# Performance work log

Measured on AMD Instinct MI355X. Metric: run time of the kernel, lower is better.

The kernel has to match this reference:

```python
import jax, jax.numpy as jnp
import numpy as np

B, F, D, H = 2048, 32, 64, 64

def setup_inputs() -> dict:
    key = jax.random.key(0)
    k1, k2, k3 = jax.random.split(key, 3)
    x = jax.random.normal(k1, (B, F, D), dtype=jnp.float32)
    W1 = jax.random.normal(k2, (D, H), dtype=jnp.float32) * 0.01
    b1 = jnp.zeros((H,), dtype=jnp.float32)
    Ws = jax.random.normal(k3, (H, 1), dtype=jnp.float32) * 0.01
    bs = jnp.zeros((1,), dtype=jnp.float32)
    return {"x": x, "W1": W1, "b1": b1, "Ws": Ws, "bs": bs}

def reference(x, W1, b1, Ws, bs):
    # pairwise field interactions: cross[b, p, d] = x[b, i_p, d] * x[b, j_p, d]
    f = x.shape[1]
    ii, jj = np.triu_indices(f, k=1)  # P = f*(f-1)/2 pairs
    cross = x[:, ii, :] * x[:, jj, :]            # [B, P, D]
    # small MLP (DNN with one hidden layer, relu, dropout disabled in eval)
    h = jax.nn.relu(jnp.einsum('bpd,dh->bph', cross, W1) + b1)  # [B, P, H]
    # attention score per pair, softmax over pairs
    scores = (jnp.einsum('bph,ho->bpo', h, Ws) + bs).squeeze(-1)  # [B, P]
    attn = jax.nn.softmax(scores, axis=-1)                        # [B, P]
    pool = jnp.sum(cross * attn[:, :, None], axis=1)              # [B, D]
    afm = jnp.sum(pool, axis=1, keepdims=True)                    # [B, 1]
    return afm
```

## Files before the change

kernel.cpp:

```cpp
#include <hip/hip_runtime.h>


#define F 32
#define D 64
#define H 64
#define P 496
#define MT 32
#define RB 72

typedef __attribute__((ext_vector_type(8))) _Float16 f16x8;
typedef __attribute__((ext_vector_type(2))) _Float16 f16x2;
typedef __attribute__((ext_vector_type(4))) float f32x4;
typedef __attribute__((ext_vector_type(2))) float f32x2;

__global__ __launch_bounds__(256, 4) void afm_kernel(
    const float* __restrict__ x, const float* __restrict__ W1,
    const float* __restrict__ b1, const float* __restrict__ Ws,
    const float* __restrict__ bs, float* __restrict__ out)
{
    __shared__ _Float16 xs[F * RB];
    __shared__ _Float16 w1f[4096];
    __shared__ float2 bw[H];
    __shared__ int pairtab[512];
    __shared__ float rednum[4], redden[4];

    const int tid  = threadIdx.x;
    const int b    = blockIdx.x;
    const int lane = tid & 63;
    const int wid  = tid >> 6;
    const int l15  = lane & 15;
    const int quad = lane >> 4;

    const float4* xb4 = (const float4*)(x + (size_t)b * (F * D));
    for (int v = tid; v < (F * D) / 4; v += 256) {
        float4 w = xb4[v];
        int row = v >> 4, col = (v & 15) * 4;
        f16x2 lo = { (_Float16)w.x, (_Float16)w.y };
        f16x2 hi = { (_Float16)w.z, (_Float16)w.w };
        *(f16x2*)&xs[row * RB + col]     = lo;
        *(f16x2*)&xs[row * RB + col + 2] = hi;
    }
    const float4* w14 = (const float4*)W1;
    #pragma unroll
    for (int s = 0; s < 4; ++s) {
        int v = tid + s * 256;
        float4 w = w14[v];
        int k  = v >> 4;
        int ks = k >> 5, kq = (k >> 3) & 3, j8 = k & 7;
        int n0 = (v & 15) * 4;
        float e4[4] = { w.x, w.y, w.z, w.w };
        #pragma unroll
        for (int c = 0; c < 4; ++c) {
            int n = n0 + c, nt = n >> 4, l = n & 15;
            w1f[(((ks * 4 + nt) * 16 + l) * 4 + kq) * 8 + j8] = (_Float16)e4[c];
        }
    }
    if (tid < H) bw[tid] = make_float2(b1[tid], Ws[tid]);
    for (int p = tid; p < 512; p += 256) {
        int i, j;
        if (p < P) {
            i = (int)((63.0f - __builtin_sqrtf((float)(3969 - 8 * p))) * 0.5f);
            if (i * (63 - i) / 2 > p) --i;
            if ((i + 1) * (62 - i) / 2 <= p) ++i;
            j = i + 1 + (p - i * (63 - i) / 2);
        } else { i = 0; j = 0; }
        pairtab[p] = (i * RB * 2) << 16 | (j * RB * 2);
    }
    const float bsv = bs[0];
    __syncthreads();

    f16x8 wfrag[4][2];
    #pragma unroll
    for (int nt = 0; nt < 4; ++nt)
        #pragma unroll
        for (int ks = 0; ks < 2; ++ks)
            wfrag[nt][ks] = *(const f16x8*)&w1f[(((ks * 4 + nt) * 16 + l15) * 4 + quad) * 8];

    const _Float16 onev = (l15 == 0) ? (_Float16)1.0f : (_Float16)0.0f;
    const f16x8 onesf = {onev, onev, onev, onev, onev, onev, onev, onev};

    f32x2 b2[8], w2[8];
    #pragma unroll
    for (int nt = 0; nt < 4; ++nt) {
        const float2* src = &bw[nt * 16 + quad * 4];
        float2 q0 = src[0], q1 = src[1], q2 = src[2], q3 = src[3];
        b2[nt*2+0] = (f32x2){q0.x, q1.x}; w2[nt*2+0] = (f32x2){q0.y, q1.y};
        b2[nt*2+1] = (f32x2){q2.x, q3.x}; w2[nt*2+1] = (f32x2){q2.y, q3.y};
    }

    const char* xsb = (const char*)xs;
    const int qb = quad << 4;
    float num = 0.f, den = 0.f;
    const f32x2 z2 = {0.f, 0.f};

    for (int t = wid; t < MT; t += 4) {
        const int p0 = t * 16;
        const int pk = pairtab[p0 + l15];
        const int io = ((unsigned)pk) >> 16;
        const int jo = pk & 0xFFFF;

        f16x8 xi0 = *(const f16x8*)(xsb + io + qb);
        f16x8 xj0 = *(const f16x8*)(xsb + jo + qb);
        f16x8 xi1 = *(const f16x8*)(xsb + io + 64 + qb);
        f16x8 xj1 = *(const f16x8*)(xsb + jo + 64 + qb);

        f16x8 A0 = xi0 * xj0;
        f16x8 A1 = xi1 * xj1;

        f32x4 acc[4];
        #pragma unroll
        for (int nt = 0; nt < 4; ++nt) { f32x4 z = {0.f,0.f,0.f,0.f}; acc[nt] = z; }
        f32x4 accs = {0.f, 0.f, 0.f, 0.f};

        #pragma unroll
        for (int nt = 0; nt < 4; ++nt)
            acc[nt] = __builtin_amdgcn_mfma_f32_16x16x32_f16(wfrag[nt][0], A0, acc[nt], 0, 0, 0);
        accs = __builtin_amdgcn_mfma_f32_16x16x32_f16(onesf, A0, accs, 0, 0, 0);
        #pragma unroll
        for (int nt = 0; nt < 4; ++nt)
            acc[nt] = __builtin_amdgcn_mfma_f32_16x16x32_f16(wfrag[nt][1], A1, acc[nt], 0, 0, 0);
        accs = __builtin_amdgcn_mfma_f32_16x16x32_f16(onesf, A1, accs, 0, 0, 0);

        f32x2 s2 = {0.f, 0.f};
        #pragma unroll
        for (int nt = 0; nt < 4; ++nt) {
            f32x2 lo = {acc[nt][0], acc[nt][1]};
            f32x2 hi = {acc[nt][2], acc[nt][3]};
            lo += b2[nt*2+0]; hi += b2[nt*2+1];
            lo = __builtin_elementwise_max(lo, z2);
            hi = __builtin_elementwise_max(hi, z2);
            s2 = lo * w2[nt*2+0] + s2;
            s2 = hi * w2[nt*2+1] + s2;
        }
        float s = s2.x + s2.y;
        s += __shfl_xor(s, 16, 64);
        s += __shfl_xor(s, 32, 64);

        float e = __expf(s + bsv);
        e = (quad == 0 && p0 + l15 < P) ? e : 0.f;
        num = fmaf(e, accs[0], num);
        den += e;
    }

    #pragma unroll
    for (int off = 8; off >= 1; off >>= 1) {
        num += __shfl_xor(num, off, 64);
        den += __shfl_xor(den, off, 64);
    }
    if (lane == 0) { rednum[wid] = num; redden[wid] = den; }
    __syncthreads();
    if (tid == 0) {
        float nn = rednum[0] + rednum[1] + rednum[2] + rednum[3];
        float dd = redden[0] + redden[1] + redden[2] + redden[3];
        out[b] = nn / dd;
    }
}

extern "C" void kernel_launch(void* const* d_in, const int* in_sizes, int n_in,
                              void* d_out, int out_size, void* d_ws, size_t ws_size,
                              hipStream_t stream) {
    const float* x  = (const float*)d_in[0];
    const float* W1 = (const float*)d_in[1];
    const float* b1 = (const float*)d_in[2];
    const float* Ws = (const float*)d_in[3];
    const float* bs = (const float*)d_in[4];
    float* out = (float*)d_out;
    const int B = in_sizes[0] / (F * D);
    afm_kernel<<<B, 256, 0, stream>>>(x, W1, b1, Ws, bs, out);
}
```

Baseline: 86.77 us.

## Process two batch rows per block to amortize weight and pair-table setup

Each block now handles two batch samples. It stages both x slices in shared memory and loops over 64 pair tiles instead of 32, so the W1 fp16 relayout, bias loads and pair-index table are built once per two samples. The bs bias is dropped from the exponent, relying on softmax shift invariance. The grid is halved, which reduces parallelism but still fills the GPU. The change also assumes B is divisible by two.

```diff
diff --git a/kernel.cpp b/kernel.cpp
--- a/kernel.cpp
+++ b/kernel.cpp
@@ -5,8 +5,8 @@
 #define D 64
 #define H 64
 #define P 496
-#define MT 32
 #define RB 72
+#define G 2
 
 typedef __attribute__((ext_vector_type(8))) _Float16 f16x8;
 typedef __attribute__((ext_vector_type(2))) _Float16 f16x2;
@@ -18,27 +18,30 @@
     const float* __restrict__ b1, const float* __restrict__ Ws,
     const float* __restrict__ bs, float* __restrict__ out)
 {
-    __shared__ _Float16 xs[F * RB];
+    __shared__ _Float16 xs[G][F * RB];
     __shared__ _Float16 w1f[4096];
     __shared__ float2 bw[H];
     __shared__ int pairtab[512];
-    __shared__ float rednum[4], redden[4];
+    __shared__ float rednum[G][4], redden[G][4];
 
     const int tid  = threadIdx.x;
-    const int b    = blockIdx.x;
     const int lane = tid & 63;
     const int wid  = tid >> 6;
     const int l15  = lane & 15;
     const int quad = lane >> 4;
+    const int b0   = blockIdx.x * G;
 
-    const float4* xb4 = (const float4*)(x + (size_t)b * (F * D));
-    for (int v = tid; v < (F * D) / 4; v += 256) {
+    const float4* xb4 = (const float4*)(x + (size_t)b0 * (F * D));
+    #pragma unroll
+    for (int s = 0; s < G * 2; ++s) {
+        int v = tid + s * 256;
         float4 w = xb4[v];
-        int row = v >> 4, col = (v & 15) * 4;
+        int g = v >> 9, idx = v & 511;
+        int row = idx >> 4, col = (idx & 15) * 4;
         f16x2 lo = { (_Float16)w.x, (_Float16)w.y };
         f16x2 hi = { (_Float16)w.z, (_Float16)w.w };
-        *(f16x2*)&xs[row * RB + col]     = lo;
-        *(f16x2*)&xs[row * RB + col + 2] = hi;
+        *(f16x2*)&xs[g][row * RB + col]     = lo;
+        *(f16x2*)&xs[g][row * RB + col + 2] = hi;
     }
     const float4* w14 = (const float4*)W1;
     #pragma unroll
@@ -66,7 +69,6 @@
         } else { i = 0; j = 0; }
         pairtab[p] = (i * RB * 2) << 16 | (j * RB * 2);
     }
-    const float bsv = bs[0];
     __syncthreads();
 
     f16x8 wfrag[4][2];
@@ -88,16 +90,19 @@
         b2[nt*2+1] = (f32x2){q2.x, q3.x}; w2[nt*2+1] = (f32x2){q2.y, q3.y};
     }
 
-    const char* xsb = (const char*)xs;
     const int qb = quad << 4;
-    float num = 0.f, den = 0.f;
+    float num[G], den[G];
+    #pragma unroll
+    for (int g = 0; g < G; ++g) { num[g] = 0.f; den[g] = 0.f; }
     const f32x2 z2 = {0.f, 0.f};
 
-    for (int t = wid; t < MT; t += 4) {
-        const int p0 = t * 16;
+    for (int t = wid; t < G * 32; t += 4) {
+        const int g  = t >> 5;
+        const int p0 = (t & 31) << 4;
         const int pk = pairtab[p0 + l15];
         const int io = ((unsigned)pk) >> 16;
         const int jo = pk & 0xFFFF;
+        const char* xsb = (const char*)xs[g];
 
         f16x8 xi0 = *(const f16x8*)(xsb + io + qb);
         f16x8 xj0 = *(const f16x8*)(xsb + jo + qb);
@@ -136,23 +141,27 @@
         s += __shfl_xor(s, 16, 64);
         s += __shfl_xor(s, 32, 64);
 
-        float e = __expf(s + bsv);
+        float e = __expf(s);
         e = (quad == 0 && p0 + l15 < P) ? e : 0.f;
-        num = fmaf(e, accs[0], num);
-        den += e;
+        num[g] = fmaf(e, accs[0], num[g]);
+        den[g] += e;
     }
 
     #pragma unroll
-    for (int off = 8; off >= 1; off >>= 1) {
-        num += __shfl_xor(num, off, 64);
-        den += __shfl_xor(den, off, 64);
+    for (int g = 0; g < G; ++g) {
+        float nn = num[g], dd = den[g];
+        #pragma unroll
+        for (int off = 8; off >= 1; off >>= 1) {
+            nn += __shfl_xor(nn, off, 64);
+            dd += __shfl_xor(dd, off, 64);
+        }
+        if (lane == 0) { rednum[g][wid] = nn; redden[g][wid] = dd; }
     }
-    if (lane == 0) { rednum[wid] = num; redden[wid] = den; }
     __syncthreads();
-    if (tid == 0) {
-        float nn = rednum[0] + rednum[1] + rednum[2] + rednum[3];
-        float dd = redden[0] + redden[1] + redden[2] + redden[3];
-        out[b] = nn / dd;
+    if (tid < G) {
+        float nn = rednum[tid][0] + rednum[tid][1] + rednum[tid][2] + rednum[tid][3];
+        float dd = redden[tid][0] + redden[tid][1] + redden[tid][2] + redden[tid][3];
+        out[b0 + tid] = nn / dd;
     }
 }
 
@@ -166,5 +175,5 @@
     const float* bs = (const float*)d_in[4];
     float* out = (float*)d_out;
     const int B = in_sizes[0] / (F * D);
-    afm_kernel<<<B, 256, 0, stream>>>(x, W1, b1, Ws, bs, out);
+    afm_kernel<<<B / G, 256, 0, stream>>>(x, W1, b1, Ws, bs, out);
 }
```

Result: no change. 85.10 us (-1.9%).

## Precompute W1 fragments and pair table once in a setup kernel

Applied to the files above, without the earlier changes.

Adds a single-block setup kernel that converts W1 to swizzled fp16, builds a per-lane pair-offset table and packs b1/Ws into workspace memory, instead of every block redoing this work. The main kernel copies the prepared W1 tile with plain int4 loads and keeps each lane's eight pair codes in registers rather than in a shared table. It also drops the scalar score bias, which cancels in the softmax, masks the last tile by index, and raises the occupancy hint to 8 blocks per CU. In exchange, each call now pays for an extra small kernel launch.

```diff
diff --git a/kernel.cpp b/kernel.cpp
--- a/kernel.cpp
+++ b/kernel.cpp
@@ -5,41 +5,26 @@
 #define D 64
 #define H 64
 #define P 496
-#define MT 32
 #define RB 72
+
+#define WS_W1F   0
+#define WS_PTAB  8192
+#define WS_BW    10240
 
 typedef __attribute__((ext_vector_type(8))) _Float16 f16x8;
 typedef __attribute__((ext_vector_type(2))) _Float16 f16x2;
 typedef __attribute__((ext_vector_type(4))) float f32x4;
 typedef __attribute__((ext_vector_type(2))) float f32x2;
 
-__global__ __launch_bounds__(256, 4) void afm_kernel(
-    const float* __restrict__ x, const float* __restrict__ W1,
-    const float* __restrict__ b1, const float* __restrict__ Ws,
-    const float* __restrict__ bs, float* __restrict__ out)
+__global__ __launch_bounds__(256) void setup_kernel(
+    const float* __restrict__ W1, const float* __restrict__ b1,
+    const float* __restrict__ Ws, void* __restrict__ ws)
 {
-    __shared__ _Float16 xs[F * RB];
-    __shared__ _Float16 w1f[4096];
-    __shared__ float2 bw[H];
-    __shared__ int pairtab[512];
-    __shared__ float rednum[4], redden[4];
+    _Float16* w1f = (_Float16*)((char*)ws + WS_W1F);
+    int* ptab     = (int*)((char*)ws + WS_PTAB);
+    float2* bwt   = (float2*)((char*)ws + WS_BW);
+    const int tid = threadIdx.x;
 
-    const int tid  = threadIdx.x;
-    const int b    = blockIdx.x;
-    const int lane = tid & 63;
-    const int wid  = tid >> 6;
-    const int l15  = lane & 15;
-    const int quad = lane >> 4;
-
-    const float4* xb4 = (const float4*)(x + (size_t)b * (F * D));
-    for (int v = tid; v < (F * D) / 4; v += 256) {
-        float4 w = xb4[v];
-        int row = v >> 4, col = (v & 15) * 4;
-        f16x2 lo = { (_Float16)w.x, (_Float16)w.y };
-        f16x2 hi = { (_Float16)w.z, (_Float16)w.w };
-        *(f16x2*)&xs[row * RB + col]     = lo;
-        *(f16x2*)&xs[row * RB + col + 2] = hi;
-    }
     const float4* w14 = (const float4*)W1;
     #pragma unroll
     for (int s = 0; s < 4; ++s) {
@@ -55,7 +40,6 @@
             w1f[(((ks * 4 + nt) * 16 + l) * 4 + kq) * 8 + j8] = (_Float16)e4[c];
         }
     }
-    if (tid < H) bw[tid] = make_float2(b1[tid], Ws[tid]);
     for (int p = tid; p < 512; p += 256) {
         int i, j;
         if (p < P) {
@@ -64,9 +48,59 @@
             if ((i + 1) * (62 - i) / 2 <= p) ++i;
             j = i + 1 + (p - i * (63 - i) / 2);
         } else { i = 0; j = 0; }
-        pairtab[p] = (i * RB * 2) << 16 | (j * RB * 2);
+        int code = (i * RB * 2) << 16 | (j * RB * 2);
+        int tile = p >> 4, l = p & 15;
+        ptab[((l * 4) + (tile & 3)) * 8 + (tile >> 2)] = code;
     }
-    const float bsv = bs[0];
+    if (tid < H) bwt[tid] = make_float2(b1[tid], Ws[tid]);
+}
+
+__global__ __launch_bounds__(256, 8) void afm_kernel(
+    const float* __restrict__ x, const void* __restrict__ ws,
+    float* __restrict__ out)
+{
+    __shared__ _Float16 xs[F * RB];
+    __shared__ _Float16 w1f[4096];
+    __shared__ float rednum[4], redden[4];
+
+    const int tid  = threadIdx.x;
+    const int b    = blockIdx.x;
+    const int lane = tid & 63;
+    const int wid  = tid >> 6;
+    const int l15  = lane & 15;
+    const int quad = lane >> 4;
+
+    const float4* xb4 = (const float4*)(x + (size_t)b * (F * D));
+    #pragma unroll
+    for (int s = 0; s < 2; ++s) {
+        int v = tid + s * 256;
+        float4 w = xb4[v];
+        int row = v >> 4, col = (v & 15) * 4;
+        f16x2 lo = { (_Float16)w.x, (_Float16)w.y };
+        f16x2 hi = { (_Float16)w.z, (_Float16)w.w };
+        *(f16x2*)&xs[row * RB + col]     = lo;
+        *(f16x2*)&xs[row * RB + col + 2] = hi;
+    }
+    const int4* wsrc = (const int4*)((const char*)ws + WS_W1F);
+    #pragma unroll
+    for (int s = 0; s < 2; ++s) {
+        int v = tid + s * 256;
+        ((int4*)w1f)[v] = wsrc[v];
+    }
+    const int4* pt4 = (const int4*)((const char*)ws + WS_PTAB);
+    int4 ca = pt4[(l15 * 4 + wid) * 2 + 0];
+    int4 cb = pt4[(l15 * 4 + wid) * 2 + 1];
+    int codes[8] = { ca.x, ca.y, ca.z, ca.w, cb.x, cb.y, cb.z, cb.w };
+
+    const float2* bwp = (const float2*)((const char*)ws + WS_BW);
+    f32x2 b2[8], w2[8];
+    #pragma unroll
+    for (int nt = 0; nt < 4; ++nt) {
+        const float2* src = &bwp[nt * 16 + quad * 4];
+        float2 q0 = src[0], q1 = src[1], q2 = src[2], q3 = src[3];
+        b2[nt*2+0] = (f32x2){q0.x, q1.x}; w2[nt*2+0] = (f32x2){q0.y, q1.y};
+        b2[nt*2+1] = (f32x2){q2.x, q3.x}; w2[nt*2+1] = (f32x2){q2.y, q3.y};
+    }
     __syncthreads();
 
     f16x8 wfrag[4][2];
@@ -79,25 +113,17 @@
     const _Float16 onev = (l15 == 0) ? (_Float16)1.0f : (_Float16)0.0f;
     const f16x8 onesf = {onev, onev, onev, onev, onev, onev, onev, onev};
 
-    f32x2 b2[8], w2[8];
-    #pragma unroll
-    for (int nt = 0; nt < 4; ++nt) {
-        const float2* src = &bw[nt * 16 + quad * 4];
-        float2 q0 = src[0], q1 = src[1], q2 = src[2], q3 = src[3];
-        b2[nt*2+0] = (f32x2){q0.x, q1.x}; w2[nt*2+0] = (f32x2){q0.y, q1.y};
-        b2[nt*2+1] = (f32x2){q2.x, q3.x}; w2[nt*2+1] = (f32x2){q2.y, q3.y};
-    }
-
     const char* xsb = (const char*)xs;
     const int qb = quad << 4;
     float num = 0.f, den = 0.f;
     const f32x2 z2 = {0.f, 0.f};
 
-    for (int t = wid; t < MT; t += 4) {
-        const int p0 = t * 16;
-        const int pk = pairtab[p0 + l15];
-        const int io = ((unsigned)pk) >> 16;
-        const int jo = pk & 0xFFFF;
+    #pragma unroll 2
+    for (int tt = 0; tt < 8; ++tt) {
+        const int t  = wid + 4 * tt;
+        const int code = codes[tt];
+        const int io = ((unsigned)code) >> 16;
+        const int jo = code & 0xFFFF;
 
         f16x8 xi0 = *(const f16x8*)(xsb + io + qb);
         f16x8 xj0 = *(const f16x8*)(xsb + jo + qb);
@@ -136,8 +162,8 @@
         s += __shfl_xor(s, 16, 64);
         s += __shfl_xor(s, 32, 64);
 
-        float e = __expf(s + bsv);
-        e = (quad == 0 && p0 + l15 < P) ? e : 0.f;
+        float e = __expf(s);
+        e = (quad == 0 && t < 31) ? e : 0.f;
         num = fmaf(e, accs[0], num);
         den += e;
     }
@@ -163,8 +189,8 @@
     const float* W1 = (const float*)d_in[1];
     const float* b1 = (const float*)d_in[2];
     const float* Ws = (const float*)d_in[3];
-    const float* bs = (const float*)d_in[4];
     float* out = (float*)d_out;
     const int B = in_sizes[0] / (F * D);
-    afm_kernel<<<B, 256, 0, stream>>>(x, W1, b1, Ws, bs, out);
+    setup_kernel<<<1, 256, 0, stream>>>(W1, b1, Ws, d_ws);
+    afm_kernel<<<B, 256, 0, stream>>>(x, d_ws, out);
 }
```

After: 277.7 us. +220.0%, slower.
